# Kernel optimization log

Hardware: AMD Instinct MI355X
Metric: run time of the kernel (lower is better)

## Reference

```python
import jax, jax.numpy as jnp
import numpy as np

T = 2.0          # hardcoded in __init__ (self.T = 2)
EPSILON = 0.1    # sinkhorn_loss default
N_ITERS = 10     # sinkhorn_loss default passed to sinkhorn_normalized
COST_CLIP = 10.0
TINY = 1e-8

B, S, V = 16, 512, 4096


def setup_inputs() -> dict:
    key = jax.random.key(0)
    k1, k2 = jax.random.split(key)
    y_s = jax.random.normal(k1, (B, S, V), dtype=jnp.float32)
    y_t = jax.random.normal(k2, (B, S, V), dtype=jnp.float32)
    return {"y_s": y_s, "y_t": y_t}


def _cdist_l1(x, y):
    # x, y: [S, V] -> [S, S]; row-streamed via lax.map to avoid a [S,S,V] intermediate
    return jax.lax.map(lambda xi: jnp.sum(jnp.abs(xi[None, :] - y), axis=-1), x)


def _sinkhorn_loss(x, y):
    # x, y: [S, V] softmax probabilities for one sample
    Wxy = _cdist_l1(x, y)                                  # [S, S]
    K = jnp.exp(-jnp.minimum(Wxy, COST_CLIP) / EPSILON)
    P = jnp.nan_to_num(K, nan=TINY, posinf=1e6, neginf=-1e6) + TINY
    for _ in range(N_ITERS):
        P = P / jnp.maximum(jnp.sum(P, axis=1, keepdims=True), TINY)
        P = jnp.nan_to_num(P, nan=TINY)
        P = P / jnp.maximum(jnp.sum(P, axis=0, keepdims=True), TINY)
        P = jnp.nan_to_num(P, nan=TINY)
    return jnp.sum(P * Wxy)


def reference(y_s, y_t):
    p_s = jax.nn.softmax(y_s / T, axis=-1)
    p_t = jax.nn.softmax(y_t / T, axis=-1)
    p_s = jnp.nan_to_num(p_s, nan=TINY)
    p_t = jnp.nan_to_num(p_t, nan=TINY)
    per_sample = jax.vmap(_sinkhorn_loss)(p_s, p_t)        # [B]
    # forward accumulates 0.001 * loss_i and divides by the number of valid samples
    return jnp.mean(0.001 * per_sample)
```

## Files before the change

kernel.cpp:

```cpp
#include <hip/hip_runtime.h>

#define B_ 16
#define S_ 512
#define V_ 4096

typedef unsigned int uint;
typedef unsigned short ushort;
typedef unsigned char u8;


__device__ __forceinline__ uint sad8(uint a, uint b, uint c) {
#if __has_builtin(__builtin_amdgcn_sad_u8)
    return __builtin_amdgcn_sad_u8(a, b, c);
#else
    uint s = c;
#pragma unroll
    for (int i = 0; i < 4; ++i) {
        uint x = (a >> (8 * i)) & 0xFFu, y = (b >> (8 * i)) & 0xFFu;
        s += x > y ? x - y : y - x;
    }
    return s;
#endif
}

__device__ __forceinline__ float bflo(uint p) { return __uint_as_float(p << 16); }
__device__ __forceinline__ float bfhi(uint p) { return __uint_as_float(p & 0xFFFF0000u); }

__device__ __forceinline__ ushort f2bf(float f) {
    uint u = __float_as_uint(f);
    u = (u + 0x7FFFu + ((u >> 16) & 1u)) >> 16;
    return (ushort)u;
}

__device__ __forceinline__ float waveMax(float v) {
#pragma unroll
    for (int o = 32; o; o >>= 1) v = fmaxf(v, __shfl_xor(v, o, 64));
    return v;
}
__device__ __forceinline__ float waveSum(float v) {
#pragma unroll
    for (int o = 32; o; o >>= 1) v += __shfl_xor(v, o, 64);
    return v;
}

#define QSCALE 65536.0f
#define QINV   1.52587890625e-5f

__global__ __launch_bounds__(256) void softmax_kernel(
        const float* __restrict__ ys, const float* __restrict__ yt,
        u8* __restrict__ qs, u8* __restrict__ qt) {
    const int row = blockIdx.x;
    const float* in = blockIdx.y ? yt : ys;
    u8* out = blockIdx.y ? qt : qs;
    const float* px = in + (size_t)row * V_;
    u8* po = out + (size_t)row * V_;
    const int tid = threadIdx.x;

    float4 v4[4];
    float m = -3.4e38f;
#pragma unroll
    for (int i = 0; i < 4; ++i) {
        v4[i] = ((const float4*)px)[tid + 256 * i];
        m = fmaxf(m, fmaxf(fmaxf(v4[i].x, v4[i].y), fmaxf(v4[i].z, v4[i].w)));
    }
    __shared__ float redm[4], reds[4];
    float wm = waveMax(m);
    if ((tid & 63) == 0) redm[tid >> 6] = wm;
    __syncthreads();
    const float rm = fmaxf(fmaxf(redm[0], redm[1]), fmaxf(redm[2], redm[3]));

    float e[16];
    float s = 0.f;
#pragma unroll
    for (int i = 0; i < 4; ++i) {
        const float* f = (const float*)&v4[i];
#pragma unroll
        for (int k = 0; k < 4; ++k) {
            float ev = __expf((f[k] - rm) * 0.5f);
            e[i * 4 + k] = ev;
            s += ev;
        }
    }
    float wsm = waveSum(s);
    if ((tid & 63) == 0) reds[tid >> 6] = wsm;
    __syncthreads();
    const float inv = 1.0f / (reds[0] + reds[1] + reds[2] + reds[3]);

#pragma unroll
    for (int i = 0; i < 4; ++i) {
        uint pk = 0;
#pragma unroll
        for (int k = 0; k < 4; ++k) {
            float p = e[i * 4 + k] * inv;
            uint q = (uint)fminf(p * QSCALE + 0.5f, 255.f);
            pk |= q << (8 * k);
        }
        ((uint*)po)[tid + 256 * i] = pk;
    }
}

#define TI 128
#define TJ 128
#define KCB 64
#define LDPB 80

__global__ __launch_bounds__(256, 4) void pairwise_kernel(
        const u8* __restrict__ qs, const u8* __restrict__ qt,
        uint* __restrict__ Acc) {
    const int bz = blockIdx.z;
    const int b = bz >> 2, vq = bz & 3;
    const int tR = blockIdx.y * TI;
    const int tC = blockIdx.x * TJ;
    const u8* xrow = qs + (size_t)b * S_ * V_ + vq * (V_ / 4);
    const u8* yrow = qt + (size_t)b * S_ * V_ + vq * (V_ / 4);
    const int tid = threadIdx.x;
    const int tx = tid & 15, ty = tid >> 4;

    __shared__ u8 xs[TI * LDPB];
    __shared__ u8 ysm[TJ * LDPB];

    const int r0 = tid >> 2, c0 = tid & 3;
    const u8* xA = xrow + (size_t)(tR + r0) * V_ + c0 * 16;
    const u8* xB = xA + (size_t)64 * V_;
    const u8* yA = yrow + (size_t)(tC + r0) * V_ + c0 * 16;
    const u8* yB = yA + (size_t)64 * V_;
    const int lw0 = r0 * LDPB + c0 * 16;
    const int lw1 = (r0 + 64) * LDPB + c0 * 16;

    uint acc[8][8];
#pragma unroll
    for (int r = 0; r < 8; ++r)
#pragma unroll
        for (int c = 0; c < 8; ++c) acc[r][c] = 0u;

    {
        uint4 a = *(const uint4*)xA, bq = *(const uint4*)xB;
        uint4 cq = *(const uint4*)yA, d = *(const uint4*)yB;
        *(uint4*)&xs[lw0] = a;  *(uint4*)&xs[lw1] = bq;
        *(uint4*)&ysm[lw0] = cq; *(uint4*)&ysm[lw1] = d;
    }
    __syncthreads();

    for (int k0 = 0; k0 < V_ / 4; k0 += KCB) {
        const int kn = k0 + KCB;
        uint4 nxA, nxB, nyA, nyB;
        const bool more = kn < V_ / 4;
        if (more) {
            nxA = *(const uint4*)(xA + kn);
            nxB = *(const uint4*)(xB + kn);
            nyA = *(const uint4*)(yA + kn);
            nyB = *(const uint4*)(yB + kn);
        }

#pragma unroll 2
        for (int kk = 0; kk < KCB; kk += 16) {
            uint4 Af[8], Bf[8];
#pragma unroll
            for (int r = 0; r < 8; ++r)
                Af[r] = *(const uint4*)&xs[(ty + 16 * r) * LDPB + kk];
#pragma unroll
            for (int c = 0; c < 8; ++c)
                Bf[c] = *(const uint4*)&ysm[(tx + 16 * c) * LDPB + kk];
#pragma unroll
            for (int r = 0; r < 8; ++r)
#pragma unroll
                for (int c = 0; c < 8; ++c) {
                    uint t = sad8(Af[r].x, Bf[c].x, acc[r][c]);
                    t = sad8(Af[r].y, Bf[c].y, t);
                    t = sad8(Af[r].z, Bf[c].z, t);
                    acc[r][c] = sad8(Af[r].w, Bf[c].w, t);
                }
        }
        __syncthreads();
        if (more) {
            *(uint4*)&xs[lw0] = nxA;  *(uint4*)&xs[lw1] = nxB;
            *(uint4*)&ysm[lw0] = nyA; *(uint4*)&ysm[lw1] = nyB;
            __syncthreads();
        }
    }

#pragma unroll
    for (int r = 0; r < 8; ++r) {
        const int i = tR + ty + 16 * r;
        const size_t base = ((size_t)b * S_ + i) * S_;
#pragma unroll
        for (int c = 0; c < 8; ++c) {
            const int j = tC + tx + 16 * c;
            atomicAdd(&Acc[base + j], acc[r][c]);
        }
    }
}

__global__ __launch_bounds__(256) void pairwise_epi(
        const uint* __restrict__ Acc, ushort* __restrict__ Wb,
        ushort* __restrict__ Kb) {
    const size_t g = (size_t)blockIdx.x * 256 + threadIdx.x;
    uint4 a = ((const uint4*)Acc)[g];
    union { uint2 u; ushort h[4]; } pw, pk;
    uint av[4] = {a.x, a.y, a.z, a.w};
#pragma unroll
    for (int t = 0; t < 4; ++t) {
        float w = fminf((float)av[t] * QINV, 10.f);
        pw.h[t] = f2bf(w);
        pk.h[t] = f2bf(__expf(-10.f * w) + 1e-8f);
    }
    ((uint2*)Wb)[g] = pw.u;
    ((uint2*)Kb)[g] = pk.u;
}

__global__ __launch_bounds__(1024) void sink_block(
        const ushort* __restrict__ Kb, const ushort* __restrict__ Wb,
        float* __restrict__ out) {
    const int b = blockIdx.x;
    const int tid = threadIdx.x, lane = tid & 63, wv = tid >> 6;
    const int ch = lane & 31, rq = lane >> 5;

    __shared__ float vp[S_];
    __shared__ float uls[S_];
    __shared__ float cwp[16][S_];
    __shared__ float redw[16];

    if (tid < S_) { vp[tid] = 1.f; uls[tid] = 1.f; }
    __syncthreads();

    const ushort* Kl = Kb + (size_t)b * S_ * S_;
    const int chB = ch * 16;

    for (int it = 0; it < 10; ++it) {
        const float4 v0 = *(const float4*)&vp[chB];
        const float4 v1 = *(const float4*)&vp[chB + 4];
        const float4 v2 = *(const float4*)&vp[chB + 8];
        const float4 v3 = *(const float4*)&vp[chB + 12];
        float4 c0 = make_float4(0.f, 0.f, 0.f, 0.f);
        float4 c1 = c0, c2 = c0, c3 = c0;

#pragma unroll 2
        for (int g = 0; g < 16; ++g) {
            const int i = wv * 32 + g * 2 + rq;
            const ushort* kp = Kl + (size_t)i * S_ + chB;
            const uint4 ka = *(const uint4*)kp;
            const uint4 kc = *(const uint4*)(kp + 8);
            float d0 = 0.f, d1 = 0.f;
            d0 = fmaf(bflo(ka.x), v0.x, d0); d0 = fmaf(bfhi(ka.x), v0.y, d0);
            d0 = fmaf(bflo(ka.y), v0.z, d0); d0 = fmaf(bfhi(ka.y), v0.w, d0);
            d0 = fmaf(bflo(ka.z), v1.x, d0); d0 = fmaf(bfhi(ka.z), v1.y, d0);
            d0 = fmaf(bflo(ka.w), v1.z, d0); d0 = fmaf(bfhi(ka.w), v1.w, d0);
            d1 = fmaf(bflo(kc.x), v2.x, d1); d1 = fmaf(bfhi(kc.x), v2.y, d1);
            d1 = fmaf(bflo(kc.y), v2.z, d1); d1 = fmaf(bfhi(kc.y), v2.w, d1);
            d1 = fmaf(bflo(kc.z), v3.x, d1); d1 = fmaf(bfhi(kc.z), v3.y, d1);
            d1 = fmaf(bflo(kc.w), v3.z, d1); d1 = fmaf(bfhi(kc.w), v3.w, d1);
            float dot = d0 + d1;
            dot += __shfl_xor(dot, 1, 64);
            dot += __shfl_xor(dot, 2, 64);
            dot += __shfl_xor(dot, 4, 64);
            dot += __shfl_xor(dot, 8, 64);
            dot += __shfl_xor(dot, 16, 64);
            const float up = uls[i];
            const float un = up / fmaxf(up * dot, 1e-8f);
            if (ch == 0) uls[i] = un;
            c0.x = fmaf(un, bflo(ka.x), c0.x); c0.y = fmaf(un, bfhi(ka.x), c0.y);
            c0.z = fmaf(un, bflo(ka.y), c0.z); c0.w = fmaf(un, bfhi(ka.y), c0.w);
            c1.x = fmaf(un, bflo(ka.z), c1.x); c1.y = fmaf(un, bfhi(ka.z), c1.y);
            c1.z = fmaf(un, bflo(ka.w), c1.z); c1.w = fmaf(un, bfhi(ka.w), c1.w);
            c2.x = fmaf(un, bflo(kc.x), c2.x); c2.y = fmaf(un, bfhi(kc.x), c2.y);
            c2.z = fmaf(un, bflo(kc.y), c2.z); c2.w = fmaf(un, bfhi(kc.y), c2.w);
            c3.x = fmaf(un, bflo(kc.z), c3.x); c3.y = fmaf(un, bfhi(kc.z), c3.y);
            c3.z = fmaf(un, bflo(kc.w), c3.z); c3.w = fmaf(un, bfhi(kc.w), c3.w);
        }
        c0.x += __shfl_xor(c0.x, 32, 64); c0.y += __shfl_xor(c0.y, 32, 64);
        c0.z += __shfl_xor(c0.z, 32, 64); c0.w += __shfl_xor(c0.w, 32, 64);
        c1.x += __shfl_xor(c1.x, 32, 64); c1.y += __shfl_xor(c1.y, 32, 64);
        c1.z += __shfl_xor(c1.z, 32, 64); c1.w += __shfl_xor(c1.w, 32, 64);
        c2.x += __shfl_xor(c2.x, 32, 64); c2.y += __shfl_xor(c2.y, 32, 64);
        c2.z += __shfl_xor(c2.z, 32, 64); c2.w += __shfl_xor(c2.w, 32, 64);
        c3.x += __shfl_xor(c3.x, 32, 64); c3.y += __shfl_xor(c3.y, 32, 64);
        c3.z += __shfl_xor(c3.z, 32, 64); c3.w += __shfl_xor(c3.w, 32, 64);
        if (rq == 0) {
            *(float4*)&cwp[wv][chB] = c0;
            *(float4*)&cwp[wv][chB + 4] = c1;
        } else {
            *(float4*)&cwp[wv][chB + 8] = c2;
            *(float4*)&cwp[wv][chB + 12] = c3;
        }
        __syncthreads();
        if (tid < S_) {
            float s = 0.f;
#pragma unroll
            for (int t = 0; t < 16; ++t) s += cwp[t][tid];
            const float vv = vp[tid];
            vp[tid] = vv / fmaxf(vv * s, 1e-8f);
        }
        __syncthreads();
    }

    const float4 v0 = *(const float4*)&vp[chB];
    const float4 v1 = *(const float4*)&vp[chB + 4];
    const float4 v2 = *(const float4*)&vp[chB + 8];
    const float4 v3 = *(const float4*)&vp[chB + 12];
    const ushort* Wl = Wb + (size_t)b * S_ * S_;
    float accl = 0.f;
#pragma unroll 2
    for (int g = 0; g < 16; ++g) {
        const int i = wv * 32 + g * 2 + rq;
        const ushort* kp = Kl + (size_t)i * S_ + chB;
        const ushort* wp = Wl + (size_t)i * S_ + chB;
        const uint4 ka = *(const uint4*)kp;
        const uint4 kc = *(const uint4*)(kp + 8);
        const uint4 wa = *(const uint4*)wp;
        const uint4 wc = *(const uint4*)(wp + 8);
        float r0 = 0.f, r1 = 0.f;
        r0 = fmaf(bflo(ka.x) * v0.x, bflo(wa.x), r0);
        r0 = fmaf(bfhi(ka.x) * v0.y, bfhi(wa.x), r0);
        r0 = fmaf(bflo(ka.y) * v0.z, bflo(wa.y), r0);
        r0 = fmaf(bfhi(ka.y) * v0.w, bfhi(wa.y), r0);
        r0 = fmaf(bflo(ka.z) * v1.x, bflo(wa.z), r0);
        r0 = fmaf(bfhi(ka.z) * v1.y, bfhi(wa.z), r0);
        r0 = fmaf(bflo(ka.w) * v1.z, bflo(wa.w), r0);
        r0 = fmaf(bfhi(ka.w) * v1.w, bfhi(wa.w), r0);
        r1 = fmaf(bflo(kc.x) * v2.x, bflo(wc.x), r1);
        r1 = fmaf(bfhi(kc.x) * v2.y, bfhi(wc.x), r1);
        r1 = fmaf(bflo(kc.y) * v2.z, bflo(wc.y), r1);
        r1 = fmaf(bfhi(kc.y) * v2.w, bfhi(wc.y), r1);
        r1 = fmaf(bflo(kc.z) * v3.x, bflo(wc.z), r1);
        r1 = fmaf(bfhi(kc.z) * v3.y, bfhi(wc.z), r1);
        r1 = fmaf(bflo(kc.w) * v3.z, bflo(wc.w), r1);
        r1 = fmaf(bfhi(kc.w) * v3.w, bfhi(wc.w), r1);
        float rp = r0 + r1;
        rp += __shfl_xor(rp, 1, 64);
        rp += __shfl_xor(rp, 2, 64);
        rp += __shfl_xor(rp, 4, 64);
        rp += __shfl_xor(rp, 8, 64);
        rp += __shfl_xor(rp, 16, 64);
        if (ch == 0) accl = fmaf(uls[i], rp, accl);
    }
    accl += __shfl_xor(accl, 32, 64);
    if (lane == 0) redw[wv] = accl;
    __syncthreads();
    if (tid == 0) {
        float s = 0.f;
#pragma unroll
        for (int t = 0; t < 16; ++t) s += redw[t];
        atomicAdd(out, s * (0.001f / 16.f));
    }
}

extern "C" void kernel_launch(void* const* d_in, const int* in_sizes, int n_in,
                              void* d_out, int out_size, void* d_ws, size_t ws_size,
                              hipStream_t stream) {
    const float* ys = (const float*)d_in[0];
    const float* yt = (const float*)d_in[1];
    float* out = (float*)d_out;

    char* w = (char*)d_ws;
    u8* qs = (u8*)w;
    u8* qt = qs + (size_t)B_ * S_ * V_;
    uint* Acc = (uint*)(qt + (size_t)B_ * S_ * V_);
    ushort* Wb = (ushort*)qs;
    ushort* Kb = Wb + (size_t)B_ * S_ * S_;

    (void)hipMemsetAsync(Acc, 0, (size_t)B_ * S_ * S_ * 4, stream);
    (void)hipMemsetAsync(out, 0, sizeof(float), stream);

    softmax_kernel<<<dim3(8192, 2), 256, 0, stream>>>(ys, yt, qs, qt);
    pairwise_kernel<<<dim3(4, 4, 64), 256, 0, stream>>>(qs, qt, Acc);
    pairwise_epi<<<4096, 256, 0, stream>>>(Acc, Wb, Kb);
    sink_block<<<16, 1024, 0, stream>>>(Kb, Wb, out);
}
```

Measured before the change: 605.3 us.

## Use direct global-to-LDS loads with double buffering and XOR swizzle in pairwise kernel

Replaces the register-staged global-to-shared copy in the L1 pairwise SAD kernel with global_load_lds direct transfers into a double-buffered LDS tile. The padded row layout gives way to an unpadded layout with an XOR swizzle on the 16-byte chunks to avoid bank conflicts. This removes one of the two barriers per K-chunk and frees the staging registers. It doubles LDS use, drops the occupancy hint in launch_bounds, and relies on the direct-to-LDS loads having finished before the single barrier.

```diff
diff --git a/kernel.cpp b/kernel.cpp
--- a/kernel.cpp
+++ b/kernel.cpp
@@ -42,6 +42,11 @@
     for (int o = 32; o; o >>= 1) v += __shfl_xor(v, o, 64);
     return v;
 }
+
+#define GLOAD_LDS16(g, l)                                                      \
+    __builtin_amdgcn_global_load_lds(                                          \
+        (const __attribute__((address_space(1))) uint*)(g),                    \
+        (__attribute__((address_space(3))) uint*)(l), 16, 0, 0)
 
 #define QSCALE 65536.0f
 #define QINV   1.52587890625e-5f
@@ -102,30 +107,29 @@
 #define TI 128
 #define TJ 128
 #define KCB 64
-#define LDPB 80
-
-__global__ __launch_bounds__(256, 4) void pairwise_kernel(
+
+__global__ __launch_bounds__(256) void pairwise_kernel(
         const u8* __restrict__ qs, const u8* __restrict__ qt,
         uint* __restrict__ Acc) {
     const int bz = blockIdx.z;
     const int b = bz >> 2, vq = bz & 3;
     const int tR = blockIdx.y * TI;
     const int tC = blockIdx.x * TJ;
-    const u8* xrow = qs + (size_t)b * S_ * V_ + vq * (V_ / 4);
-    const u8* yrow = qt + (size_t)b * S_ * V_ + vq * (V_ / 4);
+    const u8* xrow = qs + (size_t)b * S_ * V_ + vq * (V_ / 4) + (size_t)tR * V_;
+    const u8* yrow = qt + (size_t)b * S_ * V_ + vq * (V_ / 4) + (size_t)tC * V_;
     const int tid = threadIdx.x;
+    const int lane = tid & 63, wv = tid >> 6;
     const int tx = tid & 15, ty = tid >> 4;
 
-    __shared__ u8 xs[TI * LDPB];
-    __shared__ u8 ysm[TJ * LDPB];
-
-    const int r0 = tid >> 2, c0 = tid & 3;
-    const u8* xA = xrow + (size_t)(tR + r0) * V_ + c0 * 16;
-    const u8* xB = xA + (size_t)64 * V_;
-    const u8* yA = yrow + (size_t)(tC + r0) * V_ + c0 * 16;
-    const u8* yB = yA + (size_t)64 * V_;
-    const int lw0 = r0 * LDPB + c0 * 16;
-    const int lw1 = (r0 + 64) * LDPB + c0 * 16;
+    __shared__ u8 xs[2][TI * KCB];
+    __shared__ u8 ysm[2][TJ * KCB];
+
+    const int rs = lane >> 2;
+    const int coff = (((lane & 3) ^ ((lane >> 3) & 3)) << 4);
+    const size_t gs0 = (size_t)((wv * 2) * 16 + rs) * V_ + coff;
+    const size_t gs1 = (size_t)((wv * 2 + 1) * 16 + rs) * V_ + coff;
+    const int ls0 = (wv * 2) * 1024;
+    const int ls1 = (wv * 2 + 1) * 1024;
 
     uint acc[8][8];
 #pragma unroll
@@ -133,34 +137,36 @@
 #pragma unroll
         for (int c = 0; c < 8; ++c) acc[r][c] = 0u;
 
-    {
-        uint4 a = *(const uint4*)xA, bq = *(const uint4*)xB;
-        uint4 cq = *(const uint4*)yA, d = *(const uint4*)yB;
-        *(uint4*)&xs[lw0] = a;  *(uint4*)&xs[lw1] = bq;
-        *(uint4*)&ysm[lw0] = cq; *(uint4*)&ysm[lw1] = d;
-    }
-    __syncthreads();
-
-    for (int k0 = 0; k0 < V_ / 4; k0 += KCB) {
-        const int kn = k0 + KCB;
-        uint4 nxA, nxB, nyA, nyB;
-        const bool more = kn < V_ / 4;
-        if (more) {
-            nxA = *(const uint4*)(xA + kn);
-            nxB = *(const uint4*)(xB + kn);
-            nyA = *(const uint4*)(yA + kn);
-            nyB = *(const uint4*)(yB + kn);
-        }
-
-#pragma unroll 2
-        for (int kk = 0; kk < KCB; kk += 16) {
+    GLOAD_LDS16(xrow + gs0, &xs[0][ls0]);
+    GLOAD_LDS16(xrow + gs1, &xs[0][ls1]);
+    GLOAD_LDS16(yrow + gs0, &ysm[0][ls0]);
+    GLOAD_LDS16(yrow + gs1, &ysm[0][ls1]);
+    __syncthreads();
+
+    for (int c0 = 0; c0 < (V_ / 4) / KCB; ++c0) {
+        const int cur = c0 & 1;
+        if (c0 + 1 < (V_ / 4) / KCB) {
+            const int kn = (c0 + 1) * KCB;
+            GLOAD_LDS16(xrow + kn + gs0, &xs[cur ^ 1][ls0]);
+            GLOAD_LDS16(xrow + kn + gs1, &xs[cur ^ 1][ls1]);
+            GLOAD_LDS16(yrow + kn + gs0, &ysm[cur ^ 1][ls0]);
+            GLOAD_LDS16(yrow + kn + gs1, &ysm[cur ^ 1][ls1]);
+        }
+#pragma unroll
+        for (int kk = 0; kk < 4; ++kk) {
             uint4 Af[8], Bf[8];
 #pragma unroll
-            for (int r = 0; r < 8; ++r)
-                Af[r] = *(const uint4*)&xs[(ty + 16 * r) * LDPB + kk];
-#pragma unroll
-            for (int c = 0; c < 8; ++c)
-                Bf[c] = *(const uint4*)&ysm[(tx + 16 * c) * LDPB + kk];
+            for (int r = 0; r < 8; ++r) {
+                const int R = ty + 16 * r;
+                Af[r] = *(const uint4*)
+                    &xs[cur][R * KCB + ((kk ^ ((R >> 1) & 3)) << 4)];
+            }
+#pragma unroll
+            for (int c = 0; c < 8; ++c) {
+                const int C = tx + 16 * c;
+                Bf[c] = *(const uint4*)
+                    &ysm[cur][C * KCB + ((kk ^ ((C >> 1) & 3)) << 4)];
+            }
 #pragma unroll
             for (int r = 0; r < 8; ++r)
 #pragma unroll
@@ -172,11 +178,6 @@
                 }
         }
         __syncthreads();
-        if (more) {
-            *(uint4*)&xs[lw0] = nxA;  *(uint4*)&xs[lw1] = nxB;
-            *(uint4*)&ysm[lw0] = nyA; *(uint4*)&ysm[lw1] = nyB;
-            __syncthreads();
-        }
     }
 
 #pragma unroll
```

Result: faster. 548.8 us (-9.3%).
